# Kernel tuning notes

Measured on AMD Instinct MI355X. Metric: run time of the kernel, lower is better.

## Reference

```python
import jax, jax.numpy as jnp
import numpy as np

N_BOX = 20  # hardcoded boxes-per-frame in the original module


def setup_inputs() -> dict:
    key = jax.random.key(0)
    T = 256
    # boxes in [0,1); inter_area is clamped at 0 so degenerate boxes are fine,
    # and the (+1) terms in the areas keep denominators positive.
    rois = jax.random.uniform(key, (T, N_BOX, 4), dtype=jnp.float32)
    return {"rois": rois}


def reference(rois):
    # rois: [T, 20, 4] with (x1, y1, x2, y2)
    T = rois.shape[0]
    a = rois[:-1, :, None, :]  # frame t   boxes -> [T-1, 20, 1, 4]
    b = rois[1:, None, :, :]   # frame t+1 boxes -> [T-1, 1, 20, 4]

    ix1 = jnp.maximum(a[..., 0], b[..., 0])
    ix2 = jnp.minimum(a[..., 2], b[..., 2])
    iy1 = jnp.maximum(a[..., 1], b[..., 1])
    iy2 = jnp.minimum(a[..., 3], b[..., 3])
    inter = jnp.maximum(ix2 - ix1, 0.0) * jnp.maximum(iy2 - iy1, 0.0)

    area_a = (a[..., 2] - a[..., 0] + 1.0) * (a[..., 3] - a[..., 1] + 1.0)
    # faithful to source bug: second factor uses b[2]-b[1], not b[3]-b[1]
    area_b = (b[..., 2] - b[..., 0] + 1.0) * (b[..., 2] - b[..., 1] + 1.0)

    iou = inter / (area_a + area_b - inter)  # [T-1, 20, 20]

    # original writes block t at offset 20*(t-1); t=0 wraps (negative index)
    dest = (jnp.arange(T - 1) - 1) % T
    blocks = jnp.zeros((T, N_BOX, N_BOX), dtype=rois.dtype).at[dest].set(iou)

    r = jnp.arange(T)
    adj = jnp.zeros((T, N_BOX, T, N_BOX), dtype=rois.dtype)
    adj = adj.at[r, :, r, :].set(blocks)  # block-diagonal placement
    return adj.reshape(1, T * N_BOX, T * N_BOX)
```

## Files before the change

kernel.cpp:

```cpp
#include <hip/hip_runtime.h>


#define TT 256
#define NB 20
#define DIM (TT * NB)

__global__ void zero_fill_kernel(float4* __restrict__ out, int n4) {
    int idx = blockIdx.x * blockDim.x + threadIdx.x;
    int stride = gridDim.x * blockDim.x;
    float4 z = make_float4(0.f, 0.f, 0.f, 0.f);
    for (int i = idx; i < n4; i += stride) {
        out[i] = z;
    }
}

__global__ void iou_blocks_kernel(const float* __restrict__ rois,
                                  float* __restrict__ out) {
    int m = blockIdx.x;
    int k = (m == 254) ? 255 : m;
    int t = (m == 254) ? 0 : m + 1;

    __shared__ float4 A[NB];
    __shared__ float4 B[NB];
    int tid = threadIdx.x;
    if (tid < NB) {
        A[tid] = ((const float4*)rois)[t * NB + tid];
        B[tid] = ((const float4*)rois)[(t + 1) * NB + tid];
    }
    __syncthreads();

    for (int e = tid; e < NB * NB; e += blockDim.x) {
        int i = e / NB;
        int j = e % NB;
        float4 a = A[i];
        float4 b = B[j];
        float ix1 = fmaxf(a.x, b.x);
        float ix2 = fminf(a.z, b.z);
        float iy1 = fmaxf(a.y, b.y);
        float iy2 = fminf(a.w, b.w);
        float inter = fmaxf(ix2 - ix1, 0.f) * fmaxf(iy2 - iy1, 0.f);
        float area_a = (a.z - a.x + 1.f) * (a.w - a.y + 1.f);
        float area_b = (b.z - b.x + 1.f) * (b.z - b.y + 1.f);
        float iou = inter / (area_a + area_b - inter);
        size_t row = (size_t)(k * NB + i);
        size_t col = (size_t)(k * NB + j);
        out[row * DIM + col] = iou;
    }
}

extern "C" void kernel_launch(void* const* d_in, const int* in_sizes, int n_in,
                              void* d_out, int out_size, void* d_ws, size_t ws_size,
                              hipStream_t stream) {
    const float* rois = (const float*)d_in[0];
    float* out = (float*)d_out;

    int n4 = out_size / 4;
    zero_fill_kernel<<<2048, 256, 0, stream>>>((float4*)out, n4);

    iou_blocks_kernel<<<255, 128, 0, stream>>>(rois, out);
}
```

Baseline: 110.4 us.

## Fuse zero-fill and IoU block writes into one row-per-block kernel

Replaces the separate zero-fill kernel and the scattered IoU block kernel with one kernel that launches a block per output row. Each block writes its whole row with float4 stores, computing IoU values only for the diagonal 20-column segment and zeros elsewhere. This removes one kernel launch and the second pass of scattered writes over the output. The cost is that the diagonal block's rois are read redundantly by every row, and the grid is now fixed at 5120 blocks.

```diff
diff --git a/kernel.cpp b/kernel.cpp
--- a/kernel.cpp
+++ b/kernel.cpp
@@ -4,58 +4,52 @@
 #define TT 256
 #define NB 20
 #define DIM (TT * NB)
+#define DIM4 (DIM / 4)
 
-__global__ void zero_fill_kernel(float4* __restrict__ out, int n4) {
-    int idx = blockIdx.x * blockDim.x + threadIdx.x;
-    int stride = gridDim.x * blockDim.x;
-    float4 z = make_float4(0.f, 0.f, 0.f, 0.f);
-    for (int i = idx; i < n4; i += stride) {
-        out[i] = z;
-    }
-}
+__global__ void __launch_bounds__(256) fused_iou_diag_kernel(
+        const float4* __restrict__ rois, float4* __restrict__ out) {
+    int row = blockIdx.x;
+    int kr = row / NB;
+    int ri = row - kr * NB;
 
-__global__ void iou_blocks_kernel(const float* __restrict__ rois,
-                                  float* __restrict__ out) {
-    int m = blockIdx.x;
-    int k = (m == 254) ? 255 : m;
-    int t = (m == 254) ? 0 : m + 1;
+    bool active = (kr != 254);
+    int t = (kr == 255) ? 0 : kr + 1;
 
-    __shared__ float4 A[NB];
-    __shared__ float4 B[NB];
-    int tid = threadIdx.x;
-    if (tid < NB) {
-        A[tid] = ((const float4*)rois)[t * NB + tid];
-        B[tid] = ((const float4*)rois)[(t + 1) * NB + tid];
-    }
-    __syncthreads();
+    float4 a = make_float4(0.f, 0.f, 0.f, 0.f);
+    if (active) a = rois[t * NB + ri];
+    float area_a = (a.z - a.x + 1.f) * (a.w - a.y + 1.f);
 
-    for (int e = tid; e < NB * NB; e += blockDim.x) {
-        int i = e / NB;
-        int j = e % NB;
-        float4 a = A[i];
-        float4 b = B[j];
-        float ix1 = fmaxf(a.x, b.x);
-        float ix2 = fminf(a.z, b.z);
-        float iy1 = fmaxf(a.y, b.y);
-        float iy2 = fminf(a.w, b.w);
-        float inter = fmaxf(ix2 - ix1, 0.f) * fmaxf(iy2 - iy1, 0.f);
-        float area_a = (a.z - a.x + 1.f) * (a.w - a.y + 1.f);
-        float area_b = (b.z - b.x + 1.f) * (b.z - b.y + 1.f);
-        float iou = inter / (area_a + area_b - inter);
-        size_t row = (size_t)(k * NB + i);
-        size_t col = (size_t)(k * NB + j);
-        out[row * DIM + col] = iou;
+    int bcol0 = kr * (NB / 4);
+    float4* rowp = out + (size_t)row * DIM4;
+    const float4* brow = rois + (t + 1) * NB;
+
+    #pragma unroll
+    for (int it = 0; it < DIM4 / 256; ++it) {
+        int c4 = threadIdx.x + it * 256;
+        float4 v = make_float4(0.f, 0.f, 0.f, 0.f);
+        int j4 = c4 - bcol0;
+        if (active && (unsigned)j4 < (unsigned)(NB / 4)) {
+            float* vp = (float*)&v;
+            #pragma unroll
+            for (int q = 0; q < 4; ++q) {
+                float4 b = brow[j4 * 4 + q];
+                float ix1 = fmaxf(a.x, b.x);
+                float ix2 = fminf(a.z, b.z);
+                float iy1 = fmaxf(a.y, b.y);
+                float iy2 = fminf(a.w, b.w);
+                float inter = fmaxf(ix2 - ix1, 0.f) * fmaxf(iy2 - iy1, 0.f);
+                float area_b = (b.z - b.x + 1.f) * (b.z - b.y + 1.f);
+                vp[q] = inter / (area_a + area_b - inter);
+            }
+        }
+        rowp[c4] = v;
     }
 }
 
 extern "C" void kernel_launch(void* const* d_in, const int* in_sizes, int n_in,
                               void* d_out, int out_size, void* d_ws, size_t ws_size,
                               hipStream_t stream) {
-    const float* rois = (const float*)d_in[0];
-    float* out = (float*)d_out;
-
-    int n4 = out_size / 4;
-    zero_fill_kernel<<<2048, 256, 0, stream>>>((float4*)out, n4);
-
-    iou_blocks_kernel<<<255, 128, 0, stream>>>(rois, out);
+    const float4* rois = (const float4*)d_in[0];
+    float4* out = (float4*)d_out;
+    fused_iou_diag_kernel<<<DIM, 256, 0, stream>>>(rois, out);
 }
```

After: 106.8 us (median of 2 runs). -3.3%, faster.
